# Kernel optimization log

Measured on AMD Instinct MI355X. Metric: run time of the kernel, lower is better.

## Reference

```python
import jax, jax.numpy as jnp
import numpy as np

NT = 32          # nt_states
T = 64           # t_states
ST = NT + T      # total states
NEG = -1e9       # matches self.huge fill


def setup_inputs() -> dict:
    key = jax.random.key(0)
    k1, k2, k3 = jax.random.split(key, 3)
    B, n = 8, 28
    return {
        "unary_scores": jax.random.normal(k1, (B, n, T), dtype=jnp.float32),
        "rule_scores": jax.random.normal(k2, (B, NT, ST, ST), dtype=jnp.float32),
        "root_scores": jax.random.normal(k3, (B, NT), dtype=jnp.float32),
    }


def _inside(unary_scores, rule_scores, root_scores):
    # Chart indexed beta[b, width, start, state]; span (s, s+w) lives at [b, w, s].
    # Invalid (state-range) slots hold NEG, so exp() underflows them to exactly 0,
    # reproducing the terminal/nonterminal slice logic of the torch code.
    B, n, _ = unary_scores.shape
    beta = jnp.full((B, n, n, ST), NEG, dtype=unary_scores.dtype)
    beta = beta.at[:, 0, :, NT:].set(unary_scores)  # width-0 diagonal: preterminals

    mrule = rule_scores.max(axis=(2, 3))                    # [B, A]
    erule = jnp.exp(rule_scores - mrule[:, :, None, None])  # [B, A, L, R]

    for w in range(1, n):
        S = n - w                     # number of valid start positions
        k = np.arange(w)              # split offset: u = s + k
        # left child: span (s, s+k) -> width k, start s
        left = beta[:, :w, :S, :]                                  # [B, w, S, ST]
        # right child: span (s+k+1, s+w) -> width w-1-k, start s+k+1
        sr = k[:, None] + 1 + np.arange(S)[None, :]                # [w, S]
        right = beta[:, (w - 1 - k)[:, None], sr, :]               # [B, w, S, ST]

        # stable logsumexp over (k, l, r) via exp-space matmuls
        ml = left.max(-1)                                          # [B, w, S]
        mr = right.max(-1)                                         # [B, w, S]
        M = (ml + mr).max(1)                                       # [B, S]
        el = jnp.exp(left - ml[..., None])
        er = jnp.exp(right - mr[..., None] + (ml + mr - M[:, None, :])[..., None])
        numer = jnp.einsum('bksl,bksr->bslr', el, er)              # [B, S, L, R]
        total = jnp.einsum('bslr,balr->bsa', numer, erule)         # [B, S, A]
        score = jnp.log(total) + M[..., None] + mrule[:, None, :]
        beta = beta.at[:, w, :S, :NT].set(score)

    top = beta[:, n - 1, 0, :NT] + root_scores                     # span (0, n-1)
    return jax.nn.logsumexp(top, axis=1)                           # log Z, [B]


def reference(unary_scores, rule_scores, root_scores):
    return _inside(unary_scores, rule_scores, root_scores)
```

## Files before the change

kernel.cpp:

```cpp
#include <hip/hip_runtime.h>
#include <cstdint>
#include <cstddef>


#define NMAX 28

#define O_BW1 0
#define O_BMX 960
#define O_G   1744
#define O_MSP 2528
#define O_EMR 2560
#define O_NUM 2592
#define O_RED 6160
#define O_ELT 20496
#define O_ELK 6160
#define O_ERK 14480
#define O_TRI 22800
#define LDSF  34864

__device__ __forceinline__ int off32(int w, int n) {
    return (w - 1) * n - (w * (w - 1)) / 2;
}
__device__ __forceinline__ float gload(const float* p) {
    return __hip_atomic_load(p, __ATOMIC_RELAXED, __HIP_MEMORY_SCOPE_AGENT);
}
__device__ __forceinline__ void gstore(float* p, float v) {
    __hip_atomic_store(p, v, __ATOMIC_RELAXED, __HIP_MEMORY_SCOPE_AGENT);
}
__device__ __forceinline__ unsigned gloadu(const unsigned* p) {
    return __hip_atomic_load(p, __ATOMIC_RELAXED, __HIP_MEMORY_SCOPE_AGENT);
}
__device__ __forceinline__ void gstoreu(unsigned* p, unsigned v) {
    __hip_atomic_store(p, v, __ATOMIC_RELAXED, __HIP_MEMORY_SCOPE_AGENT);
}
__device__ __forceinline__ float dot4acc(float4 m, float4 t, float acc) {
    return fmaf(m.x, t.x, fmaf(m.y, t.y, fmaf(m.z, t.z, fmaf(m.w, t.w, acc))));
}

__global__ __launch_bounds__(256) void mrule_kernel(const float* __restrict__ rule,
                                                    float* __restrict__ mrule,
                                                    unsigned* __restrict__ flags) {
    int a = blockIdx.x, b = blockIdx.y, tid = threadIdx.x;
    if (a == 0 && tid < 32) gstoreu(&flags[b * 32 + tid], 0u);
    const float* base = rule + (size_t)(b * 32 + a) * 9216;
    float v = -3.0e38f;
    for (int i = tid; i < 9216; i += 256) v = fmaxf(v, base[i]);
    for (int off = 32; off > 0; off >>= 1) v = fmaxf(v, __shfl_xor(v, off, 64));
    __shared__ float red[4];
    if ((tid & 63) == 0) red[tid >> 6] = v;
    __syncthreads();
    if (tid == 0)
        mrule[b * 32 + a] = fmaxf(fmaxf(red[0], red[1]), fmaxf(red[2], red[3]));
}

__global__ __launch_bounds__(256) void pack_kernel(const float* __restrict__ rule,
                                                   const float* __restrict__ mrule,
                                                   float* __restrict__ E_TT,
                                                   float* __restrict__ E_TN,
                                                   float* __restrict__ E_NT,
                                                   float* __restrict__ E_NN) {
    int b = blockIdx.y, tid = threadIdx.x;
    int a = tid & 31;
    int cc = blockIdx.x * 8 + (tid >> 5);
    float mr = mrule[b * 32 + a];
    int l, r;
    float* dst;
    if (cc < 1024) {
        int flat = cc * 4;
        l = 32 + (flat >> 6); r = 32 + (flat & 63);
        dst = E_TT + ((size_t)(b * 1024 + cc) * 32 + a) * 4;
    } else if (cc < 1536) {
        int flat = (cc - 1024) * 4;
        l = 32 + (flat >> 5); r = flat & 31;
        dst = E_TN + ((size_t)(b * 512 + (cc - 1024)) * 32 + a) * 4;
    } else if (cc < 2048) {
        int flat = (cc - 1536) * 4;
        l = flat >> 6; r = 32 + (flat & 63);
        dst = E_NT + ((size_t)(b * 512 + (cc - 1536)) * 32 + a) * 4;
    } else {
        int flat = (cc - 2048) * 4;
        l = flat >> 5; r = flat & 31;
        dst = E_NN + ((size_t)(b * 256 + (cc - 2048)) * 32 + a) * 4;
    }
    const float4 v = *(const float4*)(rule + (((size_t)(b * 32 + a) * 96 + l) * 96 + r));
    float4 o;
    o.x = expf(v.x - mr); o.y = expf(v.y - mr);
    o.z = expf(v.z - mr); o.w = expf(v.w - mr);
    *(float4*)dst = o;
}

__global__ __launch_bounds__(1024, 4) void inside_kernel(
    const float* __restrict__ unary, const float* __restrict__ mrule,
    const float* __restrict__ E_TT, const float* __restrict__ E_TN,
    const float* __restrict__ E_NT, const float* __restrict__ E_NN,
    float* __restrict__ partA, float* __restrict__ partB,
    const float* __restrict__ root, float* __restrict__ out,
    unsigned* __restrict__ flags, int n) {
    extern __shared__ float lds[];
    const int b = blockIdx.x / 20, ch = blockIdx.x % 20;
    const int tid = threadIdx.x;
    const int a = tid & 31;

    float4 e4[2];
    {
        const float4* Eq;
        int base4;
        if (ch < 16) { Eq = (const float4*)E_TT + (size_t)b * 32768; base4 = ch * 64; }
        else         { Eq = (const float4*)E_NN + (size_t)b * 8192;  base4 = (ch - 16) * 64; }
        #pragma unroll
        for (int i = 0; i < 2; ++i)
            e4[i] = Eq[(size_t)(base4 + (tid >> 5) * 2 + i) * 32 + a];
    }
    if (tid < 32) lds[O_EMR + tid] = __expf(mrule[b * 32 + tid]);
    for (int pos = tid >> 6; pos < n; pos += 16) {
        int t = tid & 63;
        float v = unary[((size_t)b * n + pos) * 64 + t];
        float m = v;
        for (int off = 32; off > 0; off >>= 1) m = fmaxf(m, __shfl_xor(m, off, 64));
        if (t == 0) lds[O_BMX + pos] = m;
        if (ch < 16) lds[O_ELT + t * 29 + pos] = __expf(v - m);
    }
    __syncthreads();

    for (int w = 1; w < n; ++w) {
        const int S = n - w, Sp2 = S | 1;
        int q4 = (w - 2 + 3) >> 2; if (!(q4 & 1)) ++q4;
        const int K4 = 4 * q4;

        if (w >= 2) {
            if (tid < 64) {
                const unsigned tgt = (unsigned)(w - 1);
                for (;;) {
                    unsigned f = (tid < 20) ? gloadu(&flags[b * 32 + tid]) : tgt;
                    if (__ballot(f < tgt) == 0ull) break;
                    __builtin_amdgcn_s_sleep(2);
                }
            }
            __syncthreads();
        }

        const bool active = (w == 1) ? (ch < 16) : (ch < 16 || w >= 3);
        int quad, cc0;
        if (w == 1)      { quad = 0; cc0 = ch * 256; }
        else if (ch < 8) { quad = 1; cc0 = ch * 256; }
        else if (ch < 16){ quad = 2; cc0 = (ch - 8) * 256; }
        else             { quad = 3; cc0 = (ch - 16) * 256; }

        if (w >= 2) {
            const int wp = w - 1;
            const int tot = (S + 1) * 32;
            const float* pb = ((w & 1) ? partA : partB) + (size_t)b * (20 * 864);
            int e = tid;
            if (e < tot) {
                float q[20];
                #pragma unroll
                for (int c = 0; c < 20; ++c) q[c] = gload(&pb[c * 864 + e]);
                float t = (((q[0] + q[1]) + (q[2] + q[3])) + ((q[4] + q[5]) + (q[6] + q[7])))
                        + (((q[8] + q[9]) + (q[10] + q[11])) + ((q[12] + q[13]) + (q[14] + q[15])))
                        + ((q[16] + q[17]) + (q[18] + q[19]));
                int s = e >> 5, aa = e & 31;
                float t2 = t * lds[O_EMR + aa];
                float m2 = t2;
                for (int off = 16; off > 0; off >>= 1)
                    m2 = fmaxf(m2, __shfl_xor(m2, off, 32));
                float eB = t2 / m2;
                lds[O_BW1 + aa * 30 + s] = eB;
                if (ch >= 16)
                    lds[O_TRI + (off32(wp, n) + s) * 32 + aa] = eB;
                if (aa == 0)
                    lds[O_BMX + wp * NMAX + s] = __logf(m2) + lds[O_MSP + s];
            }
            if (ch >= 16 && w >= 3) {
                int idx = tid;
                if (idx < S * 32) {
                    int s = idx >> 5, sym = idx & 31;
                    int off = (sym * Sp2 + s) * K4;
                    for (int kk = 1; kk <= w - 2; ++kk)
                        lds[O_ELK + off + kk - 1] =
                            lds[O_TRI + (off32(kk, n) + s) * 32 + sym];
                    for (int k = w - 2; k < K4; ++k)
                        lds[O_ELK + off + k] = 0.f;
                }
            }
        }
        __syncthreads();

        {
            int idx = tid;
            if (idx < w * 32) {
                int k = idx >> 5, s = idx & 31;
                if (s < S) {
                    float M = -3.0e38f;
                    for (int k2 = 0; k2 < w; ++k2)
                        M = fmaxf(M, lds[O_BMX + k2 * NMAX + s] +
                                      lds[O_BMX + (w - 1 - k2) * NMAX + s + k2 + 1]);
                    lds[O_G + k * NMAX + s] =
                        __expf(lds[O_BMX + k * NMAX + s] +
                               lds[O_BMX + (w - 1 - k) * NMAX + s + k + 1] - M);
                    if (k == 0) lds[O_MSP + s] = M;
                }
            }
        }
        __syncthreads();

        if (w >= 3 && ch >= 16) {
            int idx = tid;
            if (idx < S * 32) {
                int s = idx >> 5, sym = idx & 31;
                int off = (sym * Sp2 + s) * K4;
                for (int kk = 1; kk <= w - 2; ++kk)
                    lds[O_ERK + off + kk - 1] =
                        lds[O_TRI + (off32(w - 1 - kk, n) + s + kk + 1) * 32 + sym] *
                        lds[O_G + kk * NMAX + s];
            }
            __syncthreads();
        }

        if (active) {
            const int cL = tid & 255, sh = tid >> 8;
            const int cc = cc0 + cL;
            int l, r;
            if (quad == 0 || quad == 2) { l = cc >> 6; r = cc & 63; }
            else                        { l = cc >> 5; r = cc & 31; }
            unsigned short* np = (unsigned short*)(lds + O_NUM);
            for (int s = sh; s < S; s += 4) {
                float v;
                if (quad == 0)
                    v = lds[O_ELT + l * 29 + s] * lds[O_ELT + r * 29 + (s + 1)] *
                        lds[O_G + s];
                else if (quad == 1)
                    v = lds[O_ELT + l * 29 + s] * lds[O_BW1 + r * 30 + (s + 1)] *
                        lds[O_G + s];
                else if (quad == 2)
                    v = lds[O_BW1 + l * 30 + s] * lds[O_ELT + r * 29 + (s + w)] *
                        lds[O_G + (w - 1) * NMAX + s];
                else {
                    const float* elp = lds + O_ELK + (l * Sp2 + s) * K4;
                    const float* erp = lds + O_ERK + (r * Sp2 + s) * K4;
                    float acc = 0.f;
                    for (int j = 0; j < K4; j += 4)
                        acc = dot4acc(*(const float4*)(elp + j),
                                      *(const float4*)(erp + j), acc);
                    v = acc;
                }
                unsigned u = __float_as_uint(v);
                np[s * 264 + cL] = (unsigned short)((u + 0x7fffu + ((u >> 16) & 1u)) >> 16);
            }
        }
        __syncthreads();

        if (active) {
            const char* nbase = (const char*)(lds + O_NUM);
            const int g32 = tid >> 5, wv = tid >> 6;
            const bool lowhalf = (tid & 32) == 0;
            for (int s = 0; s < S; ++s) {
                uint4 u = *(const uint4*)(nbase + s * 528 + g32 * 16);
                float acc = 0.f;
                #define LO(q) __uint_as_float((q) << 16)
                #define HI(q) __uint_as_float((q) & 0xffff0000u)
                acc = fmaf(LO(u.x), e4[0].x, acc); acc = fmaf(HI(u.x), e4[0].y, acc);
                acc = fmaf(LO(u.y), e4[0].z, acc); acc = fmaf(HI(u.y), e4[0].w, acc);
                acc = fmaf(LO(u.z), e4[1].x, acc); acc = fmaf(HI(u.z), e4[1].y, acc);
                acc = fmaf(LO(u.w), e4[1].z, acc); acc = fmaf(HI(u.w), e4[1].w, acc);
                #undef LO
                #undef HI
                acc += __shfl_xor(acc, 32, 64);
                if (lowhalf) lds[O_RED + wv * 896 + s * 32 + a] = acc;
            }
        }
        __syncthreads();

        {
            float* pb = ((w & 1) ? partB : partA) + (size_t)b * (20 * 864);
            int e = tid;
            if (e < S * 32) {
                float t = 0.f;
                if (active) {
                    #pragma unroll
                    for (int g2 = 0; g2 < 16; ++g2)
                        t += lds[O_RED + g2 * 896 + e];
                }
                gstore(&pb[ch * 864 + e], t);
            }
        }
        __syncthreads();

        if (tid == 0) gstoreu(&flags[b * 32 + ch], (unsigned)w);

        if (w == 1 && ch < 16) {
            const float4* Eq = (ch < 8)
                ? (const float4*)E_TN + (size_t)b * 16384 + (size_t)(ch * 64) * 32
                : (const float4*)E_NT + (size_t)b * 16384 + (size_t)((ch - 8) * 64) * 32;
            #pragma unroll
            for (int i = 0; i < 2; ++i)
                e4[i] = Eq[(size_t)((tid >> 5) * 2 + i) * 32 + a];
        }
    }

    if (ch == 0) {
        if (tid < 64) {
            const unsigned tgt = (unsigned)(n - 1);
            for (;;) {
                unsigned f = (tid < 20) ? gloadu(&flags[b * 32 + tid]) : tgt;
                if (__ballot(f < tgt) == 0ull) break;
                __builtin_amdgcn_s_sleep(2);
            }
        }
        __syncthreads();
        if (tid < 32) {
            const float* pb = (((n - 1) & 1) ? partB : partA) + (size_t)b * (20 * 864);
            float q[20];
            #pragma unroll
            for (int c = 0; c < 20; ++c) q[c] = gload(&pb[c * 864 + tid]);
            float t = (((q[0] + q[1]) + (q[2] + q[3])) + ((q[4] + q[5]) + (q[6] + q[7])))
                    + (((q[8] + q[9]) + (q[10] + q[11])) + ((q[12] + q[13]) + (q[14] + q[15])))
                    + ((q[16] + q[17]) + (q[18] + q[19]));
            float v = __logf(t) + lds[O_MSP + 0] + mrule[b * 32 + tid] + root[b * 32 + tid];
            float m = v;
            for (int off = 16; off > 0; off >>= 1) m = fmaxf(m, __shfl_xor(m, off, 32));
            float e = __expf(v - m);
            for (int off = 16; off > 0; off >>= 1) e += __shfl_xor(e, off, 32);
            if (tid == 0) out[b] = m + __logf(e);
        }
    }
}

extern "C" void kernel_launch(void* const* d_in, const int* in_sizes, int n_in,
                              void* d_out, int out_size, void* d_ws, size_t ws_size,
                              hipStream_t stream) {
    const float* unary = (const float*)d_in[0];
    const float* rule  = (const float*)d_in[1];
    const float* root  = (const float*)d_in[2];
    float* out = (float*)d_out;

    const int B = in_sizes[2] / 32;
    int n = in_sizes[0] / (B * 64);

    float* ws = (float*)d_ws;
    float* mrule  = ws;
    float* E_TT   = mrule + (size_t)B * 32;
    float* E_TN   = E_TT + (size_t)B * 131072;
    float* E_NT   = E_TN + (size_t)B * 65536;
    float* E_NN   = E_NT + (size_t)B * 65536;
    float* partA  = E_NN + (size_t)B * 32768;
    float* partB  = partA + (size_t)B * 20 * 864;
    unsigned* flags = (unsigned*)(partB + (size_t)B * 20 * 864);

    mrule_kernel<<<dim3(32, B), 256, 0, stream>>>(rule, mrule, flags);
    pack_kernel<<<dim3(288, B), 256, 0, stream>>>(rule, mrule, E_TT, E_TN, E_NT, E_NN);

    hipFuncSetAttribute((const void*)inside_kernel,
                        hipFuncAttributeMaxDynamicSharedMemorySize, LDSF * 4);

    void* args[] = {
        (void*)&unary, (void*)&mrule,
        (void*)&E_TT, (void*)&E_TN, (void*)&E_NT, (void*)&E_NN,
        (void*)&partA, (void*)&partB, (void*)&root,
        (void*)&out, (void*)&flags, (void*)&n
    };
    hipLaunchCooperativeKernel((void*)inside_kernel, dim3(B * 20), dim3(1024),
                               args, LDSF * 4, stream);
}
```

Measured before the change: 267.9 us.

## Decouple NN-rule blocks to lag one width behind via separate max scaling

Splits the per-batch workgroups into two roles. The 16 terminal-involving blocks advance width by width. The 4 nonterminal-nonterminal blocks run one width behind, using their own max over interior splits, which is stored in global memory and rescaled when partials are combined. This removes the dependency of the NN blocks on width w-1, so they no longer stall the critical path each step. To support the extra lag it uses a 4-slot ring of partial buffers instead of double buffering. The cost is more complex synchronisation plus extra exp and rescale work in the combine step.

```diff
diff --git a/kernel.cpp b/kernel.cpp
--- a/kernel.cpp
+++ b/kernel.cpp
@@ -4,6 +4,9 @@
 
 
 #define NMAX 28
+#define SLOT 17344
+#define MROW 17280
+#define MPROW 17312
 
 #define O_BW1 0
 #define O_BMX 960
@@ -41,7 +44,8 @@
                                                     float* __restrict__ mrule,
                                                     unsigned* __restrict__ flags) {
     int a = blockIdx.x, b = blockIdx.y, tid = threadIdx.x;
-    if (a == 0 && tid < 32) gstoreu(&flags[b * 32 + tid], 0u);
+    if (a == 0 && tid < 32)
+        gstoreu(&flags[b * 32 + tid], (tid >= 16 && tid < 20) ? 2u : 0u);
     const float* base = rule + (size_t)(b * 32 + a) * 9216;
     float v = -3.0e38f;
     for (int i = tid; i < 9216; i += 256) v = fmaxf(v, base[i]);
@@ -89,17 +93,29 @@
     *(float4*)dst = o;
 }
 
+__device__ __forceinline__ void spin_flags(const unsigned* f, unsigned tgt, int tid) {
+    if (tid < 64) {
+        for (;;) {
+            unsigned v = (tid < 20) ? gloadu(&f[tid]) : tgt;
+            if (__ballot(v < tgt) == 0ull) break;
+            __builtin_amdgcn_s_sleep(2);
+        }
+    }
+    __syncthreads();
+}
+
 __global__ __launch_bounds__(1024, 4) void inside_kernel(
     const float* __restrict__ unary, const float* __restrict__ mrule,
     const float* __restrict__ E_TT, const float* __restrict__ E_TN,
     const float* __restrict__ E_NT, const float* __restrict__ E_NN,
-    float* __restrict__ partA, float* __restrict__ partB,
-    const float* __restrict__ root, float* __restrict__ out,
-    unsigned* __restrict__ flags, int n) {
+    float* __restrict__ part, const float* __restrict__ root,
+    float* __restrict__ out, unsigned* __restrict__ flags, int n) {
     extern __shared__ float lds[];
     const int b = blockIdx.x / 20, ch = blockIdx.x % 20;
     const int tid = threadIdx.x;
     const int a = tid & 31;
+    unsigned* const myflags = flags + b * 32;
+    float* const pbase = part + (size_t)(b * 4) * SLOT;
 
     float4 e4[2];
     {
@@ -122,205 +138,255 @@
     }
     __syncthreads();
 
-    for (int w = 1; w < n; ++w) {
-        const int S = n - w, Sp2 = S | 1;
-        int q4 = (w - 2 + 3) >> 2; if (!(q4 & 1)) ++q4;
-        const int K4 = 4 * q4;
-
-        if (w >= 2) {
-            if (tid < 64) {
-                const unsigned tgt = (unsigned)(w - 1);
-                for (;;) {
-                    unsigned f = (tid < 20) ? gloadu(&flags[b * 32 + tid]) : tgt;
-                    if (__ballot(f < tgt) == 0ull) break;
-                    __builtin_amdgcn_s_sleep(2);
-                }
-            }
-            __syncthreads();
+    if (ch < 16) {
+        for (int w = 1; w < n; ++w) {
+            const int S = n - w;
+            float* pbW = pbase + (size_t)(w & 3) * SLOT;
+
+            if (w >= 2) {
+                spin_flags(myflags, (unsigned)(w - 1), tid);
+                const int wp = w - 1;
+                const float* pbP = pbase + (size_t)(wp & 3) * SLOT;
+                if (tid < (S + 1) * 32) {
+                    int s = tid >> 5, aa = tid & 31;
+                    float q[20];
+                    #pragma unroll
+                    for (int c = 0; c < 20; ++c) q[c] = gload(&pbP[c * 864 + tid]);
+                    float tT = (((q[0] + q[1]) + (q[2] + q[3])) + ((q[4] + q[5]) + (q[6] + q[7])))
+                             + (((q[8] + q[9]) + (q[10] + q[11])) + ((q[12] + q[13]) + (q[14] + q[15])));
+                    float t = tT;
+                    if (wp >= 3) {
+                        float tN = (q[16] + q[17]) + (q[18] + q[19]);
+                        float Mp = gload(&pbP[MPROW + s]);
+                        t = fmaf(__expf(Mp - lds[O_MSP + s]), tN, tT);
+                    }
+                    float t2 = t * lds[O_EMR + aa];
+                    float m2 = t2;
+                    for (int off = 16; off > 0; off >>= 1)
+                        m2 = fmaxf(m2, __shfl_xor(m2, off, 32));
+                    lds[O_BW1 + aa * 30 + s] = t2 / m2;
+                    if (aa == 0)
+                        lds[O_BMX + wp * NMAX + s] = __logf(m2) + lds[O_MSP + s];
+                }
+                __syncthreads();
+            }
+
+            if (tid < S) {
+                int s = tid;
+                float M = -3.0e38f;
+                for (int k = 0; k < w; ++k)
+                    M = fmaxf(M, lds[O_BMX + k * NMAX + s] +
+                                  lds[O_BMX + (w - 1 - k) * NMAX + s + k + 1]);
+                lds[O_MSP + s] = M;
+                lds[O_G + s] =
+                    __expf(lds[O_BMX + s] + lds[O_BMX + (w - 1) * NMAX + s + 1] - M);
+                lds[O_G + NMAX + s] =
+                    __expf(lds[O_BMX + (w - 1) * NMAX + s] + lds[O_BMX + s + w] - M);
+                if (ch == 0) gstore(&pbW[MROW + s], M);
+            }
+            __syncthreads();
+
+            {
+                const int cL = tid & 255, sh = tid >> 8;
+                const bool tn = (w >= 2) && (ch < 8);
+                const int cc = (w == 1) ? ch * 256 + cL
+                             : (ch < 8 ? ch * 256 + cL : (ch - 8) * 256 + cL);
+                int l, r;
+                if (tn) { l = cc >> 5; r = cc & 31; }
+                else    { l = cc >> 6; r = cc & 63; }
+                unsigned short* np = (unsigned short*)(lds + O_NUM);
+                for (int s = sh; s < S; s += 4) {
+                    float v;
+                    if (w == 1)
+                        v = lds[O_ELT + l * 29 + s] * lds[O_ELT + r * 29 + (s + 1)] *
+                            lds[O_G + s];
+                    else if (tn)
+                        v = lds[O_ELT + l * 29 + s] * lds[O_BW1 + r * 30 + (s + 1)] *
+                            lds[O_G + s];
+                    else
+                        v = lds[O_BW1 + l * 30 + s] * lds[O_ELT + r * 29 + (s + w)] *
+                            lds[O_G + NMAX + s];
+                    unsigned u = __float_as_uint(v);
+                    np[s * 264 + cL] = (unsigned short)((u + 0x7fffu + ((u >> 16) & 1u)) >> 16);
+                }
+            }
+            __syncthreads();
+
+            {
+                const char* nbase = (const char*)(lds + O_NUM);
+                const int g32 = tid >> 5, wv = tid >> 6;
+                const bool lowhalf = (tid & 32) == 0;
+                for (int s = 0; s < S; ++s) {
+                    uint4 u = *(const uint4*)(nbase + s * 528 + g32 * 16);
+                    float acc = 0.f;
+                    #define LO(q) __uint_as_float((q) << 16)
+                    #define HI(q) __uint_as_float((q) & 0xffff0000u)
+                    acc = fmaf(LO(u.x), e4[0].x, acc); acc = fmaf(HI(u.x), e4[0].y, acc);
+                    acc = fmaf(LO(u.y), e4[0].z, acc); acc = fmaf(HI(u.y), e4[0].w, acc);
+                    acc = fmaf(LO(u.z), e4[1].x, acc); acc = fmaf(HI(u.z), e4[1].y, acc);
+                    acc = fmaf(LO(u.w), e4[1].z, acc); acc = fmaf(HI(u.w), e4[1].w, acc);
+                    #undef LO
+                    #undef HI
+                    acc += __shfl_xor(acc, 32, 64);
+                    if (lowhalf) lds[O_RED + wv * 896 + s * 32 + a] = acc;
+                }
+            }
+            __syncthreads();
+
+            if (tid < S * 32) {
+                float t = 0.f;
+                #pragma unroll
+                for (int g2 = 0; g2 < 16; ++g2) t += lds[O_RED + g2 * 896 + tid];
+                gstore(&pbW[ch * 864 + tid], t);
+            }
+            __syncthreads();
+            if (tid == 0) gstoreu(&myflags[ch], (unsigned)w);
+
+            if (w == 1) {
+                const float4* Eq = (ch < 8)
+                    ? (const float4*)E_TN + (size_t)b * 16384 + (size_t)(ch * 64) * 32
+                    : (const float4*)E_NT + (size_t)b * 16384 + (size_t)((ch - 8) * 64) * 32;
+                #pragma unroll
+                for (int i = 0; i < 2; ++i)
+                    e4[i] = Eq[(size_t)((tid >> 5) * 2 + i) * 32 + a];
+            }
         }
 
-        const bool active = (w == 1) ? (ch < 16) : (ch < 16 || w >= 3);
-        int quad, cc0;
-        if (w == 1)      { quad = 0; cc0 = ch * 256; }
-        else if (ch < 8) { quad = 1; cc0 = ch * 256; }
-        else if (ch < 16){ quad = 2; cc0 = (ch - 8) * 256; }
-        else             { quad = 3; cc0 = (ch - 16) * 256; }
-
-        if (w >= 2) {
-            const int wp = w - 1;
-            const int tot = (S + 1) * 32;
-            const float* pb = ((w & 1) ? partA : partB) + (size_t)b * (20 * 864);
-            int e = tid;
-            if (e < tot) {
+        if (ch == 0) {
+            spin_flags(myflags, (unsigned)(n - 1), tid);
+            if (tid < 32) {
+                const float* pbP = pbase + (size_t)((n - 1) & 3) * SLOT;
                 float q[20];
                 #pragma unroll
-                for (int c = 0; c < 20; ++c) q[c] = gload(&pb[c * 864 + e]);
-                float t = (((q[0] + q[1]) + (q[2] + q[3])) + ((q[4] + q[5]) + (q[6] + q[7])))
-                        + (((q[8] + q[9]) + (q[10] + q[11])) + ((q[12] + q[13]) + (q[14] + q[15])))
-                        + ((q[16] + q[17]) + (q[18] + q[19]));
-                int s = e >> 5, aa = e & 31;
-                float t2 = t * lds[O_EMR + aa];
-                float m2 = t2;
-                for (int off = 16; off > 0; off >>= 1)
-                    m2 = fmaxf(m2, __shfl_xor(m2, off, 32));
-                float eB = t2 / m2;
-                lds[O_BW1 + aa * 30 + s] = eB;
-                if (ch >= 16)
-                    lds[O_TRI + (off32(wp, n) + s) * 32 + aa] = eB;
-                if (aa == 0)
-                    lds[O_BMX + wp * NMAX + s] = __logf(m2) + lds[O_MSP + s];
-            }
-            if (ch >= 16 && w >= 3) {
-                int idx = tid;
-                if (idx < S * 32) {
-                    int s = idx >> 5, sym = idx & 31;
-                    int off = (sym * Sp2 + s) * K4;
-                    for (int kk = 1; kk <= w - 2; ++kk)
-                        lds[O_ELK + off + kk - 1] =
-                            lds[O_TRI + (off32(kk, n) + s) * 32 + sym];
-                    for (int k = w - 2; k < K4; ++k)
-                        lds[O_ELK + off + k] = 0.f;
-                }
+                for (int c = 0; c < 20; ++c) q[c] = gload(&pbP[c * 864 + tid]);
+                float tT = (((q[0] + q[1]) + (q[2] + q[3])) + ((q[4] + q[5]) + (q[6] + q[7])))
+                         + (((q[8] + q[9]) + (q[10] + q[11])) + ((q[12] + q[13]) + (q[14] + q[15])));
+                float tN = (q[16] + q[17]) + (q[18] + q[19]);
+                float Mp = gload(&pbP[MPROW + 0]);
+                float t = fmaf(__expf(Mp - lds[O_MSP + 0]), tN, tT);
+                float v = __logf(t) + lds[O_MSP + 0] + mrule[b * 32 + tid] + root[b * 32 + tid];
+                float m = v;
+                for (int off = 16; off > 0; off >>= 1) m = fmaxf(m, __shfl_xor(m, off, 32));
+                float e = __expf(v - m);
+                for (int off = 16; off > 0; off >>= 1) e += __shfl_xor(e, off, 32);
+                if (tid == 0) out[b] = m + __logf(e);
             }
         }
-        __syncthreads();
-
-        {
-            int idx = tid;
-            if (idx < w * 32) {
-                int k = idx >> 5, s = idx & 31;
+    } else {
+        for (int w = 3; w < n; ++w) {
+            const int S = n - w, Sp2 = S | 1;
+            int q4 = (w - 2 + 3) >> 2; if (!(q4 & 1)) ++q4;
+            const int K4 = 4 * q4;
+            float* pbW = pbase + (size_t)(w & 3) * SLOT;
+
+            spin_flags(myflags, (unsigned)(w - 2), tid);
+
+            {
+                const int wf = w - 2;
+                const float* pbF = pbase + (size_t)(wf & 3) * SLOT;
+                if (tid < (n - wf) * 32) {
+                    int s = tid >> 5, aa = tid & 31;
+                    float q[20];
+                    #pragma unroll
+                    for (int c = 0; c < 20; ++c) q[c] = gload(&pbF[c * 864 + tid]);
+                    float tT = (((q[0] + q[1]) + (q[2] + q[3])) + ((q[4] + q[5]) + (q[6] + q[7])))
+                             + (((q[8] + q[9]) + (q[10] + q[11])) + ((q[12] + q[13]) + (q[14] + q[15])));
+                    float Mf = gload(&pbF[MROW + s]);
+                    float t = tT;
+                    if (wf >= 3) {
+                        float tN = (q[16] + q[17]) + (q[18] + q[19]);
+                        float Mp = gload(&pbF[MPROW + s]);
+                        t = fmaf(__expf(Mp - Mf), tN, tT);
+                    }
+                    float t2 = t * lds[O_EMR + aa];
+                    float m2 = t2;
+                    for (int off = 16; off > 0; off >>= 1)
+                        m2 = fmaxf(m2, __shfl_xor(m2, off, 32));
+                    lds[O_TRI + (off32(wf, n) + s) * 32 + aa] = t2 / m2;
+                    if (aa == 0) lds[O_BMX + wf * NMAX + s] = __logf(m2) + Mf;
+                }
+                __syncthreads();
+            }
+
+            if (tid < (w - 2) * 32) {
+                int k = (tid >> 5) + 1, s = tid & 31;
                 if (s < S) {
-                    float M = -3.0e38f;
-                    for (int k2 = 0; k2 < w; ++k2)
-                        M = fmaxf(M, lds[O_BMX + k2 * NMAX + s] +
-                                      lds[O_BMX + (w - 1 - k2) * NMAX + s + k2 + 1]);
+                    float Mp = -3.0e38f;
+                    for (int k2 = 1; k2 <= w - 2; ++k2)
+                        Mp = fmaxf(Mp, lds[O_BMX + k2 * NMAX + s] +
+                                       lds[O_BMX + (w - 1 - k2) * NMAX + s + k2 + 1]);
                     lds[O_G + k * NMAX + s] =
                         __expf(lds[O_BMX + k * NMAX + s] +
-                               lds[O_BMX + (w - 1 - k) * NMAX + s + k + 1] - M);
-                    if (k == 0) lds[O_MSP + s] = M;
-                }
-            }
-        }
-        __syncthreads();
-
-        if (w >= 3 && ch >= 16) {
-            int idx = tid;
-            if (idx < S * 32) {
-                int s = idx >> 5, sym = idx & 31;
+                               lds[O_BMX + (w - 1 - k) * NMAX + s + k + 1] - Mp);
+                    if (k == 1 && ch == 16) gstore(&pbW[MPROW + s], Mp);
+                }
+            }
+            __syncthreads();
+
+            if (tid < S * 32) {
+                int s = tid >> 5, sym = tid & 31;
                 int off = (sym * Sp2 + s) * K4;
-                for (int kk = 1; kk <= w - 2; ++kk)
+                for (int kk = 1; kk <= w - 2; ++kk) {
+                    lds[O_ELK + off + kk - 1] =
+                        lds[O_TRI + (off32(kk, n) + s) * 32 + sym];
                     lds[O_ERK + off + kk - 1] =
                         lds[O_TRI + (off32(w - 1 - kk, n) + s + kk + 1) * 32 + sym] *
                         lds[O_G + kk * NMAX + s];
-            }
-            __syncthreads();
-        }
-
-        if (active) {
-            const int cL = tid & 255, sh = tid >> 8;
-            const int cc = cc0 + cL;
-            int l, r;
-            if (quad == 0 || quad == 2) { l = cc >> 6; r = cc & 63; }
-            else                        { l = cc >> 5; r = cc & 31; }
-            unsigned short* np = (unsigned short*)(lds + O_NUM);
-            for (int s = sh; s < S; s += 4) {
-                float v;
-                if (quad == 0)
-                    v = lds[O_ELT + l * 29 + s] * lds[O_ELT + r * 29 + (s + 1)] *
-                        lds[O_G + s];
-                else if (quad == 1)
-                    v = lds[O_ELT + l * 29 + s] * lds[O_BW1 + r * 30 + (s + 1)] *
-                        lds[O_G + s];
-                else if (quad == 2)
-                    v = lds[O_BW1 + l * 30 + s] * lds[O_ELT + r * 29 + (s + w)] *
-                        lds[O_G + (w - 1) * NMAX + s];
-                else {
+                }
+                for (int k = w - 2; k < K4; ++k) {
+                    lds[O_ELK + off + k] = 0.f;
+                    lds[O_ERK + off + k] = 0.f;
+                }
+            }
+            __syncthreads();
+
+            {
+                const int cL = tid & 255, sh = tid >> 8;
+                const int cc = (ch - 16) * 256 + cL;
+                const int l = cc >> 5, r = cc & 31;
+                unsigned short* np = (unsigned short*)(lds + O_NUM);
+                for (int s = sh; s < S; s += 4) {
                     const float* elp = lds + O_ELK + (l * Sp2 + s) * K4;
                     const float* erp = lds + O_ERK + (r * Sp2 + s) * K4;
                     float acc = 0.f;
                     for (int j = 0; j < K4; j += 4)
                         acc = dot4acc(*(const float4*)(elp + j),
                                       *(const float4*)(erp + j), acc);
-                    v = acc;
-                }
-                unsigned u = __float_as_uint(v);
-                np[s * 264 + cL] = (unsigned short)((u + 0x7fffu + ((u >> 16) & 1u)) >> 16);
-            }
-        }
-        __syncthreads();
-
-        if (active) {
-            const char* nbase = (const char*)(lds + O_NUM);
-            const int g32 = tid >> 5, wv = tid >> 6;
-            const bool lowhalf = (tid & 32) == 0;
-            for (int s = 0; s < S; ++s) {
-                uint4 u = *(const uint4*)(nbase + s * 528 + g32 * 16);
-                float acc = 0.f;
-                #define LO(q) __uint_as_float((q) << 16)
-                #define HI(q) __uint_as_float((q) & 0xffff0000u)
-                acc = fmaf(LO(u.x), e4[0].x, acc); acc = fmaf(HI(u.x), e4[0].y, acc);
-                acc = fmaf(LO(u.y), e4[0].z, acc); acc = fmaf(HI(u.y), e4[0].w, acc);
-                acc = fmaf(LO(u.z), e4[1].x, acc); acc = fmaf(HI(u.z), e4[1].y, acc);
-                acc = fmaf(LO(u.w), e4[1].z, acc); acc = fmaf(HI(u.w), e4[1].w, acc);
-                #undef LO
-                #undef HI
-                acc += __shfl_xor(acc, 32, 64);
-                if (lowhalf) lds[O_RED + wv * 896 + s * 32 + a] = acc;
-            }
-        }
-        __syncthreads();
-
-        {
-            float* pb = ((w & 1) ? partB : partA) + (size_t)b * (20 * 864);
-            int e = tid;
-            if (e < S * 32) {
+                    unsigned u = __float_as_uint(acc);
+                    np[s * 264 + cL] = (unsigned short)((u + 0x7fffu + ((u >> 16) & 1u)) >> 16);
+                }
+            }
+            __syncthreads();
+
+            {
+                const char* nbase = (const char*)(lds + O_NUM);
+                const int g32 = tid >> 5, wv = tid >> 6;
+                const bool lowhalf = (tid & 32) == 0;
+                for (int s = 0; s < S; ++s) {
+                    uint4 u = *(const uint4*)(nbase + s * 528 + g32 * 16);
+                    float acc = 0.f;
+                    #define LO(q) __uint_as_float((q) << 16)
+                    #define HI(q) __uint_as_float((q) & 0xffff0000u)
+                    acc = fmaf(LO(u.x), e4[0].x, acc); acc = fmaf(HI(u.x), e4[0].y, acc);
+                    acc = fmaf(LO(u.y), e4[0].z, acc); acc = fmaf(HI(u.y), e4[0].w, acc);
+                    acc = fmaf(LO(u.z), e4[1].x, acc); acc = fmaf(HI(u.z), e4[1].y, acc);
+                    acc = fmaf(LO(u.w), e4[1].z, acc); acc = fmaf(HI(u.w), e4[1].w, acc);
+                    #undef LO
+                    #undef HI
+                    acc += __shfl_xor(acc, 32, 64);
+                    if (lowhalf) lds[O_RED + wv * 896 + s * 32 + a] = acc;
+                }
+            }
+            __syncthreads();
+
+            if (tid < S * 32) {
                 float t = 0.f;
-                if (active) {
-                    #pragma unroll
-                    for (int g2 = 0; g2 < 16; ++g2)
-                        t += lds[O_RED + g2 * 896 + e];
-                }
-                gstore(&pb[ch * 864 + e], t);
-            }
-        }
-        __syncthreads();
-
-        if (tid == 0) gstoreu(&flags[b * 32 + ch], (unsigned)w);
-
-        if (w == 1 && ch < 16) {
-            const float4* Eq = (ch < 8)
-                ? (const float4*)E_TN + (size_t)b * 16384 + (size_t)(ch * 64) * 32
-                : (const float4*)E_NT + (size_t)b * 16384 + (size_t)((ch - 8) * 64) * 32;
-            #pragma unroll
-            for (int i = 0; i < 2; ++i)
-                e4[i] = Eq[(size_t)((tid >> 5) * 2 + i) * 32 + a];
-        }
-    }
-
-    if (ch == 0) {
-        if (tid < 64) {
-            const unsigned tgt = (unsigned)(n - 1);
-            for (;;) {
-                unsigned f = (tid < 20) ? gloadu(&flags[b * 32 + tid]) : tgt;
-                if (__ballot(f < tgt) == 0ull) break;
-                __builtin_amdgcn_s_sleep(2);
-            }
-        }
-        __syncthreads();
-        if (tid < 32) {
-            const float* pb = (((n - 1) & 1) ? partB : partA) + (size_t)b * (20 * 864);
-            float q[20];
-            #pragma unroll
-            for (int c = 0; c < 20; ++c) q[c] = gload(&pb[c * 864 + tid]);
-            float t = (((q[0] + q[1]) + (q[2] + q[3])) + ((q[4] + q[5]) + (q[6] + q[7])))
-                    + (((q[8] + q[9]) + (q[10] + q[11])) + ((q[12] + q[13]) + (q[14] + q[15])))
-                    + ((q[16] + q[17]) + (q[18] + q[19]));
-            float v = __logf(t) + lds[O_MSP + 0] + mrule[b * 32 + tid] + root[b * 32 + tid];
-            float m = v;
-            for (int off = 16; off > 0; off >>= 1) m = fmaxf(m, __shfl_xor(m, off, 32));
-            float e = __expf(v - m);
-            for (int off = 16; off > 0; off >>= 1) e += __shfl_xor(e, off, 32);
-            if (tid == 0) out[b] = m + __logf(e);
+                #pragma unroll
+                for (int g2 = 0; g2 < 16; ++g2) t += lds[O_RED + g2 * 896 + tid];
+                gstore(&pbW[ch * 864 + tid], t);
+            }
+            __syncthreads();
+            if (tid == 0) gstoreu(&myflags[ch], (unsigned)w);
         }
     }
 }
@@ -342,9 +408,8 @@
     float* E_TN   = E_TT + (size_t)B * 131072;
     float* E_NT   = E_TN + (size_t)B * 65536;
     float* E_NN   = E_NT + (size_t)B * 65536;
-    float* partA  = E_NN + (size_t)B * 32768;
-    float* partB  = partA + (size_t)B * 20 * 864;
-    unsigned* flags = (unsigned*)(partB + (size_t)B * 20 * 864);
+    float* part   = E_NN + (size_t)B * 32768;
+    unsigned* flags = (unsigned*)(part + (size_t)B * 4 * SLOT);
 
     mrule_kernel<<<dim3(32, B), 256, 0, stream>>>(rule, mrule, flags);
     pack_kernel<<<dim3(288, B), 256, 0, stream>>>(rule, mrule, E_TT, E_TN, E_NT, E_NN);
@@ -355,8 +420,7 @@
     void* args[] = {
         (void*)&unary, (void*)&mrule,
         (void*)&E_TT, (void*)&E_TN, (void*)&E_NT, (void*)&E_NN,
-        (void*)&partA, (void*)&partB, (void*)&root,
-        (void*)&out, (void*)&flags, (void*)&n
+        (void*)&part, (void*)&root, (void*)&out, (void*)&flags, (void*)&n
     };
     hipLaunchCooperativeKernel((void*)inside_kernel, dim3(B * 20), dim3(1024),
                                args, LDSF * 4, stream);
```

Result: faster. 242.7 us (-9.4%).
